# Optimization experiments

Hardware: AMD Instinct MI355X
Metric: run time of the kernel (lower is better)

Reference implementation:

```python
import jax, jax.numpy as jnp
import numpy as np

MAX_TAG = 16          # tag ids live in [0, MAX_TAG]; 0 = background
NUM_SEG = MAX_TAG + 1
LGG_VALUE = 3.0


def setup_inputs() -> dict:
    key = jax.random.key(0)
    k1, k2, k3 = jax.random.split(key, 3)
    B, C, H, W = 16, 8, 512, 512
    gt_kernel_key = jax.random.randint(k1, (B, H, W), 0, MAX_TAG + 1, dtype=jnp.int32)
    training_mask = jax.random.randint(k2, (B, H, W), 0, 2, dtype=jnp.int32)
    similarity_vector = jax.random.normal(k3, (B, C, H, W), dtype=jnp.float32)
    return {
        "gt_kernel_key": gt_kernel_key,
        "training_mask": training_mask,
        "similarity_vector": similarity_vector,
    }


def _per_sample_loss(sim_hwc, gk, mask):
    # sim_hwc: [H, W, C]; gk, mask: [H, W]
    C = sim_hwc.shape[-1]
    flat_sim = sim_hwc.reshape(-1, C)            # [HW, C]
    flat_gk = gk.reshape(-1)                     # [HW]
    ones = jnp.ones_like(flat_gk, dtype=jnp.float32)

    # segment mean per tag over the UNMASKED kernel map (matches original:
    # tags are selected with the mask, but means use gt_kernel directly)
    sums = jax.ops.segment_sum(flat_sim, flat_gk, num_segments=NUM_SEG)      # [T, C]
    counts = jax.ops.segment_sum(ones, flat_gk, num_segments=NUM_SEG)       # [T]
    means = sums / jnp.maximum(counts, 1.0)[:, None]

    # a tag participates iff it appears in gt_kernel_key * training_mask and != 0
    masked_gk = flat_gk * mask.reshape(-1)
    masked_counts = jax.ops.segment_sum(ones, masked_gk, num_segments=NUM_SEG)
    present = (masked_counts > 0).at[0].set(False)                           # [T]

    # pairwise distances between tag means (tiny: NUM_SEG x NUM_SEG)
    diff = means[:, None, :] - means[None, :, :]                             # [T, T, C]
    dist = jnp.sqrt(jnp.sum(diff * diff, axis=-1) + 1e-12)                   # [T, T]
    pair_loss = jnp.log(jnp.maximum(LGG_VALUE - dist, 0.0) ** 2 + 1.0)

    valid = present[:, None] & present[None, :] & ~jnp.eye(NUM_SEG, dtype=bool)
    n_valid = jnp.sum(valid.astype(jnp.float32))
    loss = jnp.sum(jnp.where(valid, pair_loss, 0.0)) / jnp.maximum(n_valid, 1.0)
    sample_valid = (jnp.sum(present.astype(jnp.int32)) >= 2).astype(jnp.float32)
    return loss, sample_valid


def reference(gt_kernel_key, training_mask, similarity_vector):
    # [B, C, H, W] -> [B, H, W, C]
    sim = jnp.transpose(similarity_vector, (0, 2, 3, 1))
    losses, valids = jax.vmap(_per_sample_loss)(sim, gt_kernel_key, training_mask)
    n = jnp.sum(valids)
    return jnp.where(n > 0, jnp.sum(losses * valids) / jnp.maximum(n, 1.0), 0.0)
```

## Files before the change

kernel.cpp:

```cpp
#include <hip/hip_runtime.h>

#define NB 16
#define NC 8
#define HW (512*512)
#define NT 16
#define LGG 3.0f

#define BLOCKS 2048
#define THREADS 256
#define BPSAMP (BLOCKS/NB)
#define PXB (HW/BPSAMP)
#define PXW (PXB/4)
#define NMFMA (PXW/32)
#define NCOL 10
#define ACCW (NT*NCOL)

typedef __attribute__((ext_vector_type(8))) short bf16x8;
typedef __attribute__((ext_vector_type(4))) float f32x4;


__device__ __forceinline__ unsigned pk_bf16(float x, float y) {
    unsigned r;
    asm("v_cvt_pk_bf16_f32 %0, %1, %2" : "=v"(r) : "v"(x), "v"(y));
    return r;
}

__global__ __launch_bounds__(256) void init_ws(float* g_acc) {
    const int i = threadIdx.x;
    #pragma unroll
    for (int k = 0; k < NB*ACCW; k += 256)
        if (k + i < NB*ACCW) g_acc[k + i] = 0.f;
}

__global__ __launch_bounds__(THREADS) void accum(
    const int* __restrict__ gk, const int* __restrict__ mask,
    const float* __restrict__ sim, float* __restrict__ g_acc)
{
    const int tid  = threadIdx.x;
    const int lane = tid & 63, wid = tid >> 6;
    const int bid  = blockIdx.x;
    const int b    = bid / BPSAMP;
    const int sb   = bid % BPSAMP;
    const int c    = lane & 15;
    const int l4   = lane >> 4;
    const int p0   = sb * PXB + wid * PXW + l4 * 8;

    const int*   gkp = gk   + (size_t)b * HW + p0;
    const int*   mkp = mask + (size_t)b * HW + p0;
    const float* sp  = sim  + ((size_t)b * NC + c) * HW + p0;

    __shared__ float lred[4][256];

    f32x4 acc = {0.f, 0.f, 0.f, 0.f};
    const int r1 = c + 1;

    #pragma unroll 2
    for (int it = 0; it < NMFMA; ++it) {
        const int off = it * 32;
        const int4 g0 = *(const int4*)(gkp + off);
        const int4 g1 = *(const int4*)(gkp + off + 4);

        union { bf16x8 v; unsigned u[4]; } A;
        A.u[0] = (g0.x == r1 ? 0x3F80u : 0u) | (g0.y == r1 ? 0x3F800000u : 0u);
        A.u[1] = (g0.z == r1 ? 0x3F80u : 0u) | (g0.w == r1 ? 0x3F800000u : 0u);
        A.u[2] = (g1.x == r1 ? 0x3F80u : 0u) | (g1.y == r1 ? 0x3F800000u : 0u);
        A.u[3] = (g1.z == r1 ? 0x3F80u : 0u) | (g1.w == r1 ? 0x3F800000u : 0u);

        union { bf16x8 v; unsigned u[4]; } B;
        if (c < 8) {
            const float4 v0 = *(const float4*)(sp + off);
            const float4 v1 = *(const float4*)(sp + off + 4);
            B.u[0] = pk_bf16(v0.x, v0.y); B.u[1] = pk_bf16(v0.z, v0.w);
            B.u[2] = pk_bf16(v1.x, v1.y); B.u[3] = pk_bf16(v1.z, v1.w);
        } else if (c == 8) {
            B.u[0] = B.u[1] = B.u[2] = B.u[3] = 0x3F803F80u;
        } else if (c == 9) {
            const int4 m0 = *(const int4*)(mkp + off);
            const int4 m1 = *(const int4*)(mkp + off + 4);
            B.u[0] = (m0.x ? 0x3F80u : 0u) | (m0.y ? 0x3F800000u : 0u);
            B.u[1] = (m0.z ? 0x3F80u : 0u) | (m0.w ? 0x3F800000u : 0u);
            B.u[2] = (m1.x ? 0x3F80u : 0u) | (m1.y ? 0x3F800000u : 0u);
            B.u[3] = (m1.z ? 0x3F80u : 0u) | (m1.w ? 0x3F800000u : 0u);
        } else {
            B.u[0] = B.u[1] = B.u[2] = B.u[3] = 0u;
        }

        acc = __builtin_amdgcn_mfma_f32_16x16x32_bf16(A.v, B.v, acc, 0, 0, 0);
    }

    const int row0 = (lane >> 4) * 4;
    #pragma unroll
    for (int i = 0; i < 4; ++i) lred[wid][(row0 + i) * 16 + c] = acc[i];
    __syncthreads();

    if (tid < NT * NCOL) {
        const int r = tid / NCOL, cc = tid % NCOL;
        const float s = lred[0][r*16+cc] + lred[1][r*16+cc]
                      + lred[2][r*16+cc] + lred[3][r*16+cc];
        atomicAdd(&g_acc[b * ACCW + tid], s);
    }
}

__global__ __launch_bounds__(256) void finalize(
    const float* __restrict__ g_acc, float* __restrict__ out)
{
    __shared__ float    means[NB][NT][NC];
    __shared__ unsigned pres[NB];
    __shared__ float    sl[NB], sn[NB];
    const int tid = threadIdx.x;

    if (tid < NB) pres[tid] = 0u;
    __syncthreads();

    {
        const int b = tid >> 4, t = tid & 15;
        const float* row = g_acc + b * ACCW + t * NCOL;
        const float cnt = row[8];
        const float mc  = row[9];
        const float inv = 1.f / fmaxf(cnt, 1.f);
        #pragma unroll
        for (int cc = 0; cc < NC; ++cc) means[b][t][cc] = row[cc] * inv;
        if (mc > 0.5f) atomicOr(&pres[b], 1u << (t + 1));
    }
    __syncthreads();

    const int b = tid >> 4, i = tid & 15;
    const unsigned pr = pres[b];
    float loss = 0.f, nv = 0.f;
    if ((pr >> (i + 1)) & 1u) {
        #pragma unroll
        for (int j = 0; j < NT; ++j) {
            if (j != i && ((pr >> (j + 1)) & 1u)) {
                float d2 = 0.f;
                #pragma unroll
                for (int cc = 0; cc < NC; ++cc) {
                    const float d = means[b][i][cc] - means[b][j][cc];
                    d2 += d * d;
                }
                const float dist = sqrtf(d2 + 1e-12f);
                const float r = fmaxf(LGG - dist, 0.f);
                loss += logf(r * r + 1.f);
                nv += 1.f;
            }
        }
    }
    #pragma unroll
    for (int o = 8; o; o >>= 1) { loss += __shfl_xor(loss, o); nv += __shfl_xor(nv, o); }
    if (i == 0) {
        const float v = (__popc(pr) >= 2) ? 1.f : 0.f;
        sl[b] = v * (loss / fmaxf(nv, 1.f));
        sn[b] = v;
    }
    __syncthreads();
    if (tid == 0) {
        float tl = 0.f, tv = 0.f;
        for (int bb = 0; bb < NB; ++bb) { tl += sl[bb]; tv += sn[bb]; }
        out[0] = (tv > 0.f) ? tl / tv : 0.f;
    }
}

extern "C" void kernel_launch(void* const* d_in, const int* in_sizes, int n_in,
                              void* d_out, int out_size, void* d_ws, size_t ws_size,
                              hipStream_t stream) {
    const int*   gk   = (const int*)d_in[0];
    const int*   mask = (const int*)d_in[1];
    const float* sim  = (const float*)d_in[2];
    float* out   = (float*)d_out;
    float* g_acc = (float*)d_ws;

    init_ws<<<1, 256, 0, stream>>>(g_acc);
    accum<<<BLOCKS, THREADS, 0, stream>>>(gk, mask, sim, g_acc);
    finalize<<<1, 256, 0, stream>>>(g_acc, out);
}
```

Baseline: 54.71 us.

## Software-pipeline accum loads with a triple-buffered register prefetch and branchless select

Restructures the accumulation loop so global loads for iteration it+2 are issued before computing iteration it, using a three-deep register ring of fragments and a fully unrolled loop. All lanes now load gk, mask and sim unconditionally and choose the B operand with selects instead of divergent branches, clamping the channel index so lanes 8-15 read valid sim addresses. This aims to hide memory latency and remove wave divergence. In exchange it issues redundant mask and sim loads on most lanes and raises register pressure, which launch_bounds(256,1) permits.

```diff
diff --git a/kernel.cpp b/kernel.cpp
--- a/kernel.cpp
+++ b/kernel.cpp
@@ -18,11 +18,48 @@
 typedef __attribute__((ext_vector_type(8))) short bf16x8;
 typedef __attribute__((ext_vector_type(4))) float f32x4;
 
-
 __device__ __forceinline__ unsigned pk_bf16(float x, float y) {
     unsigned r;
     asm("v_cvt_pk_bf16_f32 %0, %1, %2" : "=v"(r) : "v"(x), "v"(y));
     return r;
+}
+
+struct Frag { int4 g0, g1, m0, m1; float4 v0, v1; };
+
+__device__ __forceinline__ Frag ld(const int* gkp, const int* mkp,
+                                   const float* sp, int off) {
+    Frag f;
+    f.g0 = *(const int4*)(gkp + off);
+    f.g1 = *(const int4*)(gkp + off + 4);
+    f.m0 = *(const int4*)(mkp + off);
+    f.m1 = *(const int4*)(mkp + off + 4);
+    f.v0 = *(const float4*)(sp + off);
+    f.v1 = *(const float4*)(sp + off + 4);
+    return f;
+}
+
+__device__ __forceinline__ unsigned onehot2(int a, int b, int r1) {
+    return (a == r1 ? 0x3F80u : 0u) | (b == r1 ? 0x3F800000u : 0u);
+}
+__device__ __forceinline__ unsigned mask2(int a, int b) {
+    return (a ? 0x3F80u : 0u) | (b ? 0x3F800000u : 0u);
+}
+
+__device__ __forceinline__ f32x4 step(const Frag& f, int c, int r1, f32x4 acc) {
+    union { bf16x8 v; unsigned u[4]; } A, B;
+    A.u[0] = onehot2(f.g0.x, f.g0.y, r1);
+    A.u[1] = onehot2(f.g0.z, f.g0.w, r1);
+    A.u[2] = onehot2(f.g1.x, f.g1.y, r1);
+    A.u[3] = onehot2(f.g1.z, f.g1.w, r1);
+    const unsigned bs0 = pk_bf16(f.v0.x, f.v0.y), bs1 = pk_bf16(f.v0.z, f.v0.w);
+    const unsigned bs2 = pk_bf16(f.v1.x, f.v1.y), bs3 = pk_bf16(f.v1.z, f.v1.w);
+    const unsigned bm0 = mask2(f.m0.x, f.m0.y), bm1 = mask2(f.m0.z, f.m0.w);
+    const unsigned bm2 = mask2(f.m1.x, f.m1.y), bm3 = mask2(f.m1.z, f.m1.w);
+    B.u[0] = c < 8 ? bs0 : (c == 8 ? 0x3F803F80u : (c == 9 ? bm0 : 0u));
+    B.u[1] = c < 8 ? bs1 : (c == 8 ? 0x3F803F80u : (c == 9 ? bm1 : 0u));
+    B.u[2] = c < 8 ? bs2 : (c == 8 ? 0x3F803F80u : (c == 9 ? bm2 : 0u));
+    B.u[3] = c < 8 ? bs3 : (c == 8 ? 0x3F803F80u : (c == 9 ? bm3 : 0u));
+    return __builtin_amdgcn_mfma_f32_16x16x32_bf16(A.v, B.v, acc, 0, 0, 0);
 }
 
 __global__ __launch_bounds__(256) void init_ws(float* g_acc) {
@@ -32,7 +69,7 @@
         if (k + i < NB*ACCW) g_acc[k + i] = 0.f;
 }
 
-__global__ __launch_bounds__(THREADS) void accum(
+__global__ __launch_bounds__(THREADS, 1) void accum(
     const int* __restrict__ gk, const int* __restrict__ mask,
     const float* __restrict__ sim, float* __restrict__ g_acc)
 {
@@ -47,45 +84,21 @@
 
     const int*   gkp = gk   + (size_t)b * HW + p0;
     const int*   mkp = mask + (size_t)b * HW + p0;
-    const float* sp  = sim  + ((size_t)b * NC + c) * HW + p0;
+    const float* sp  = sim  + ((size_t)b * NC + (c & 7)) * HW + p0;
 
     __shared__ float lred[4][256];
 
     f32x4 acc = {0.f, 0.f, 0.f, 0.f};
     const int r1 = c + 1;
 
-    #pragma unroll 2
+    Frag fr[3];
+    fr[0] = ld(gkp, mkp, sp, 0);
+    fr[1] = ld(gkp, mkp, sp, 32);
+    #pragma unroll
     for (int it = 0; it < NMFMA; ++it) {
-        const int off = it * 32;
-        const int4 g0 = *(const int4*)(gkp + off);
-        const int4 g1 = *(const int4*)(gkp + off + 4);
-
-        union { bf16x8 v; unsigned u[4]; } A;
-        A.u[0] = (g0.x == r1 ? 0x3F80u : 0u) | (g0.y == r1 ? 0x3F800000u : 0u);
-        A.u[1] = (g0.z == r1 ? 0x3F80u : 0u) | (g0.w == r1 ? 0x3F800000u : 0u);
-        A.u[2] = (g1.x == r1 ? 0x3F80u : 0u) | (g1.y == r1 ? 0x3F800000u : 0u);
-        A.u[3] = (g1.z == r1 ? 0x3F80u : 0u) | (g1.w == r1 ? 0x3F800000u : 0u);
-
-        union { bf16x8 v; unsigned u[4]; } B;
-        if (c < 8) {
-            const float4 v0 = *(const float4*)(sp + off);
-            const float4 v1 = *(const float4*)(sp + off + 4);
-            B.u[0] = pk_bf16(v0.x, v0.y); B.u[1] = pk_bf16(v0.z, v0.w);
-            B.u[2] = pk_bf16(v1.x, v1.y); B.u[3] = pk_bf16(v1.z, v1.w);
-        } else if (c == 8) {
-            B.u[0] = B.u[1] = B.u[2] = B.u[3] = 0x3F803F80u;
-        } else if (c == 9) {
-            const int4 m0 = *(const int4*)(mkp + off);
-            const int4 m1 = *(const int4*)(mkp + off + 4);
-            B.u[0] = (m0.x ? 0x3F80u : 0u) | (m0.y ? 0x3F800000u : 0u);
-            B.u[1] = (m0.z ? 0x3F80u : 0u) | (m0.w ? 0x3F800000u : 0u);
-            B.u[2] = (m1.x ? 0x3F80u : 0u) | (m1.y ? 0x3F800000u : 0u);
-            B.u[3] = (m1.z ? 0x3F80u : 0u) | (m1.w ? 0x3F800000u : 0u);
-        } else {
-            B.u[0] = B.u[1] = B.u[2] = B.u[3] = 0u;
-        }
-
-        acc = __builtin_amdgcn_mfma_f32_16x16x32_bf16(A.v, B.v, acc, 0, 0, 0);
+        if (it + 2 < NMFMA)
+            fr[(it + 2) % 3] = ld(gkp, mkp, sp, (it + 2) * 32);
+        acc = step(fr[it % 3], c, r1, acc);
     }
 
     const int row0 = (lane >> 4) * 4;
```

New measurement: 60.95 us. +11.4%, slower.
